# Optimization experiments

Measured on AMD Instinct MI355X. Metric: run time of the kernel, lower is better.

The kernel has to match this reference:

```python
import jax, jax.numpy as jnp
import numpy as np

B, N, D = 2, 8192, 1024
H = 16
HD = D // H  # 64
EPS = 1e-6


def setup_inputs() -> dict:
    key = jax.random.key(0)
    ks = jax.random.split(key, 5)
    scale = 1.0 / np.sqrt(D)
    return {
        "x": jax.random.normal(ks[0], (B, N, D), dtype=jnp.float32),
        "Wq": jax.random.normal(ks[1], (D, D), dtype=jnp.float32) * scale,
        "Wk": jax.random.normal(ks[2], (D, D), dtype=jnp.float32) * scale,
        "Wv": jax.random.normal(ks[3], (D, D), dtype=jnp.float32) * scale,
        "Wo": jax.random.normal(ks[4], (D, D), dtype=jnp.float32) * scale,
    }


def _feature_map(a):
    # ELU + 1 (positive feature map)
    return jax.nn.elu(a) + 1.0


def reference(x, Wq, Wk, Wv, Wo):
    b, n, d = x.shape
    # torch nn.Linear: y = x @ W.T
    q = _feature_map((x @ Wq.T).reshape(b, n, H, HD))  # (B,N,H,hd)
    k = _feature_map((x @ Wk.T).reshape(b, n, H, HD))
    v = (x @ Wv.T).reshape(b, n, H, HD)
    # global kv state per head: (B,H,hd,hd)
    kv = jnp.einsum('bnhd,bnhm->bhdm', k, v)
    k_sum = k.sum(axis=1)  # (B,H,hd)
    numerator = jnp.einsum('bnhd,bhdm->bnhm', q, kv)  # (B,N,H,hd)
    denominator = jnp.einsum('bnhd,bhd->bnh', q, k_sum)[..., None]
    out = numerator / (denominator + EPS)
    out = out.reshape(b, n, d)
    return out @ Wo.T
```

## Files before the change

### kernel.cpp

```cpp
#include <hip/hip_runtime.h>
#include <stdint.h>

#define BB 2
#define NN 8192
#define DD 1024
#define KK 1024
#define NHEAD 16
#define HDIM 64
#define KV_CHUNKS 32

using f32x4  = __attribute__((ext_vector_type(4))) float;
using bf16x8 = __attribute__((ext_vector_type(8))) short;

__device__ __forceinline__ unsigned short f2bf(float f) {
  union { float f; unsigned int u; } v; v.f = f;
  unsigned int r = v.u + 0x7fffu + ((v.u >> 16) & 1u);
  return (unsigned short)(r >> 16);
}
__device__ __forceinline__ float bf2f(unsigned short u) {
  union { unsigned int u; float f; } v; v.u = ((unsigned int)u) << 16;
  return v.f;
}

__device__ __forceinline__ void gload_lds16(const unsigned short* g, unsigned short* l) {
  __builtin_amdgcn_global_load_lds(
      (__attribute__((address_space(1))) void*)(const_cast<unsigned short*>(g)),
      (__attribute__((address_space(3))) void*)(l), 16, 0, 0);
}

__global__ __launch_bounds__(256) void f32_to_bf16_k(const float* __restrict__ in,
                                                     unsigned short* __restrict__ out) {
  size_t i = ((size_t)blockIdx.x * 256 + threadIdx.x) * 8;
  float4 a = *(const float4*)(in + i);
  float4 b = *(const float4*)(in + i + 4);
  uint32_t p0 = (uint32_t)f2bf(a.x) | ((uint32_t)f2bf(a.y) << 16);
  uint32_t p1 = (uint32_t)f2bf(a.z) | ((uint32_t)f2bf(a.w) << 16);
  uint32_t p2 = (uint32_t)f2bf(b.x) | ((uint32_t)f2bf(b.y) << 16);
  uint32_t p3 = (uint32_t)f2bf(b.z) | ((uint32_t)f2bf(b.w) << 16);
  *(uint4*)(out + i) = make_uint4(p0, p1, p2, p3);
}

#define BAR  __builtin_amdgcn_s_barrier()
#define SB   __builtin_amdgcn_sched_barrier(0)
#define WLG  asm volatile("s_waitcnt lgkmcnt(0)" ::: "memory")
#define WVM4 asm volatile("s_waitcnt vmcnt(4)" ::: "memory")
#define WVM0 asm volatile("s_waitcnt vmcnt(0)" ::: "memory")

template <int EPI>
__global__ __launch_bounds__(512, 2) void gemm256(const unsigned short* __restrict__ A,
                                                  const unsigned short* __restrict__ Bw,
                                                  unsigned short* __restrict__ O0,
                                                  unsigned short* __restrict__ O1,
                                                  unsigned short* __restrict__ O2,
                                                  float* __restrict__ OF) {
  __shared__ unsigned short lds[2][2][2][128 * 64];
  const int t = threadIdx.x;
  const int lane = t & 63;
  const int w = t >> 6;
  const int wm = w >> 2;
  const int wn = w & 3;
  const int frow = lane & 15;
  const int g = lane >> 4;
  const int fx = frow & 7;
  const int rowBase = blockIdx.x * 256;
  const int colBase = blockIdx.y * 256;

  const int srow0 = t >> 3;
  const int ssw = ((t & 7) ^ (srow0 & 7)) * 8;
  const unsigned short* sA0 = A + (size_t)(rowBase + srow0) * KK + ssw;
  const unsigned short* sA1 = A + (size_t)(rowBase + 64 + srow0) * KK + ssw;
  const unsigned short* sB0 = Bw + (size_t)(colBase + srow0) * KK + ssw;
  const unsigned short* sB1 = Bw + (size_t)(colBase + 64 + srow0) * KK + ssw;

#define STAGE(db, ab, half, kt)                                                        \
  do {                                                                                 \
    gload_lds16(((ab) ? sB0 : sA0) + (size_t)(half) * 128 * KK + (size_t)(kt) * 64,    \
                &lds[db][ab][half][(0 * 512 + w * 64) * 8]);                           \
    gload_lds16(((ab) ? sB1 : sA1) + (size_t)(half) * 128 * KK + (size_t)(kt) * 64,    \
                &lds[db][ab][half][(1 * 512 + w * 64) * 8]);                           \
  } while (0)

  bf16x8 ar[4][2], br[4][2];
  f32x4 acc[8][4];
#pragma unroll
  for (int i = 0; i < 8; ++i)
#pragma unroll
    for (int j = 0; j < 4; ++j) acc[i][j] = (f32x4){0.f, 0.f, 0.f, 0.f};

#define LDA4(db, mih)                                                                  \
  _Pragma("unroll") for (int mi2 = 0; mi2 < 4; ++mi2)                                  \
  _Pragma("unroll") for (int kk2 = 0; kk2 < 2; ++kk2)                                  \
    ar[mi2][kk2] = *(const bf16x8*)((const char*)&lds[db][0][wm][0] +                  \
        ((mih) * 64 + mi2 * 16 + frow) * 128 + ((kk2 * 4 + g) ^ fx) * 16);

#define LDB2(db, nih)                                                                  \
  _Pragma("unroll") for (int ni2 = 0; ni2 < 2; ++ni2)                                  \
  _Pragma("unroll") for (int kk2 = 0; kk2 < 2; ++kk2)                                  \
    br[(nih) * 2 + ni2][kk2] = *(const bf16x8*)((const char*)&lds[db][1][wn >> 1][0] + \
        ((wn & 1) * 64 + (nih) * 32 + ni2 * 16 + frow) * 128 + ((kk2 * 4 + g) ^ fx) * 16);

#define MFMAQ(mih, nih)                                                                \
  __builtin_amdgcn_s_setprio(1);                                                      \
  _Pragma("unroll") for (int mi2 = 0; mi2 < 4; ++mi2)                                  \
  _Pragma("unroll") for (int ni2 = 0; ni2 < 2; ++ni2)                                  \
  _Pragma("unroll") for (int kk2 = 0; kk2 < 2; ++kk2)                                  \
    acc[(mih) * 4 + mi2][(nih) * 2 + ni2] = __builtin_amdgcn_mfma_f32_16x16x32_bf16(   \
        ar[mi2][kk2], br[(nih) * 2 + ni2][kk2],                                        \
        acc[(mih) * 4 + mi2][(nih) * 2 + ni2], 0, 0, 0);                               \
  __builtin_amdgcn_s_setprio(0);

  STAGE(0, 1, 0, 0); STAGE(0, 1, 1, 0);
  STAGE(0, 0, 0, 0); STAGE(0, 0, 1, 0);
  STAGE(1, 1, 0, 1); STAGE(1, 1, 1, 1);
  WVM4; BAR; SB;

#pragma unroll 1
  for (int i = 0; i < 8; ++i) {
    const bool full = (i < 7);
    const int kt1 = 2 * i + 1, kt2 = 2 * i + 2, kt3 = 2 * i + 3;
    LDA4(0, 0); LDB2(0, 0);
    STAGE(1, 0, 0, kt1);
    BAR; WLG; SB; MFMAQ(0, 0); BAR; SB;
    LDB2(0, 1);
    STAGE(1, 0, 1, kt1);
    BAR; WLG; SB; MFMAQ(0, 1); BAR; SB;
    LDA4(0, 1);
    if (full) STAGE(0, 1, 0, kt2);
    BAR; WLG; SB; MFMAQ(1, 0); BAR; SB;
    if (full) { STAGE(0, 1, 1, kt2); WVM4; } else { WVM0; }
    BAR; SB; MFMAQ(1, 1); BAR; SB;
    LDA4(1, 0); LDB2(1, 0);
    if (full) STAGE(0, 0, 0, kt2);
    BAR; WLG; SB; MFMAQ(0, 0); BAR; SB;
    LDB2(1, 1);
    if (full) STAGE(0, 0, 1, kt2);
    BAR; WLG; SB; MFMAQ(0, 1); BAR; SB;
    LDA4(1, 1);
    if (full) STAGE(1, 1, 0, kt3);
    BAR; WLG; SB; MFMAQ(1, 0); BAR; SB;
    if (full) { STAGE(1, 1, 1, kt3); WVM4; }
    BAR; SB; MFMAQ(1, 1); BAR; SB;
  }

  const int r0 = rowBase + wm * 128 + g * 4;
  if constexpr (EPI == 0) {
    const int ymat = blockIdx.y >> 2;
    unsigned short* dst = (ymat == 0) ? O0 : ((ymat == 1) ? O1 : O2);
    const int c0 = (blockIdx.y & 3) * 256 + wn * 64 + frow;
    const bool doElu = (ymat < 2);
#pragma unroll
    for (int mi = 0; mi < 8; ++mi)
#pragma unroll
      for (int j = 0; j < 4; ++j) {
        const size_t ro = (size_t)(r0 + mi * 16 + j) * DD;
#pragma unroll
        for (int ni = 0; ni < 4; ++ni) {
          float v = acc[mi][ni][j];
          if (doElu) v = (v > 0.f) ? (v + 1.f) : __expf(v);
          dst[ro + c0 + ni * 16] = f2bf(v);
        }
      }
  } else {
    const int c0 = colBase + wn * 64 + frow;
#pragma unroll
    for (int mi = 0; mi < 8; ++mi)
#pragma unroll
      for (int j = 0; j < 4; ++j) {
        const size_t ro = (size_t)(r0 + mi * 16 + j) * DD;
#pragma unroll
        for (int ni = 0; ni < 4; ++ni)
          OF[ro + c0 + ni * 16] = acc[mi][ni][j];
      }
  }
#undef STAGE
#undef LDA4
#undef LDB2
#undef MFMAQ
}

__global__ __launch_bounds__(256) void kv_partial(const unsigned short* __restrict__ Kb,
                                                  const unsigned short* __restrict__ Vb,
                                                  float* __restrict__ kvp,
                                                  float* __restrict__ ksp) {
  __shared__ unsigned short ks[16][64];
  __shared__ float vsf[16][64];
  const int blk = blockIdx.x;
  const int c = blk % KV_CHUNKS;
  const int h = (blk / KV_CHUNKS) % NHEAD;
  const int b = blk / (KV_CHUNKS * NHEAD);
  const int chunkLen = NN / KV_CHUNKS;
  const int t = threadIdx.x;
  const int d = t >> 2;
  const int mq = (t & 3) * 16;
  float acc[16] = {};
  float sk = 0.f;
  const size_t base = ((size_t)b * NN + (size_t)c * chunkLen) * DD + h * HDIM;
  const int half = t >> 7;
  const int tt = t & 127;
  const int rr = tt >> 3;
  const int cc = (tt & 7) * 8;
  const unsigned short* src0 = (half ? Vb : Kb) + base + (size_t)rr * DD + cc;
  for (int n0 = 0; n0 < chunkLen; n0 += 16) {
    uint4 raw = *(const uint4*)(src0 + (size_t)n0 * DD);
    if (half == 0) {
      *(uint4*)&ks[rr][cc] = raw;
    } else {
      const unsigned short* pr = (const unsigned short*)&raw;
      float4 f0, f1;
      f0.x = bf2f(pr[0]); f0.y = bf2f(pr[1]); f0.z = bf2f(pr[2]); f0.w = bf2f(pr[3]);
      f1.x = bf2f(pr[4]); f1.y = bf2f(pr[5]); f1.z = bf2f(pr[6]); f1.w = bf2f(pr[7]);
      *(float4*)&vsf[rr][cc] = f0;
      *(float4*)&vsf[rr][cc + 4] = f1;
    }
    __syncthreads();
#pragma unroll
    for (int nn = 0; nn < 16; ++nn) {
      float kd = bf2f(ks[nn][d]);
      sk += kd;
      const float4* vrow = (const float4*)&vsf[nn][mq];
#pragma unroll
      for (int j4 = 0; j4 < 4; ++j4) {
        float4 vv = vrow[j4];
        acc[j4 * 4 + 0] += kd * vv.x;
        acc[j4 * 4 + 1] += kd * vv.y;
        acc[j4 * 4 + 2] += kd * vv.z;
        acc[j4 * 4 + 3] += kd * vv.w;
      }
    }
    __syncthreads();
  }
  float* dst = kvp + (size_t)blk * 4096 + d * 64 + mq;
#pragma unroll
  for (int j = 0; j < 16; ++j) dst[j] = acc[j];
  if ((t & 3) == 0) ksp[(size_t)blk * 64 + d] = sk;
}

__global__ __launch_bounds__(256) void kv_final(const float* __restrict__ kvp,
                                                const float* __restrict__ ksp,
                                                unsigned short* __restrict__ kvb) {
  const int bh = blockIdx.x;
  const int t = threadIdx.x;
  __shared__ float kvs[4096];
#pragma unroll
  for (int e0 = 0; e0 < 4096; e0 += 256) {
    float s = 0.f;
    for (int cI = 0; cI < KV_CHUNKS; ++cI)
      s += kvp[((size_t)bh * KV_CHUNKS + cI) * 4096 + e0 + t];
    kvs[e0 + t] = s;
  }
  __syncthreads();
  unsigned short* dst = kvb + (size_t)bh * (96 * 64);
#pragma unroll
  for (int e0 = 0; e0 < 4096; e0 += 256) {
    int e = e0 + t;
    dst[e] = f2bf(kvs[(e & 63) * 64 + (e >> 6)]);
  }
  if (t < 64) {
    float s = 0.f;
    for (int cI = 0; cI < KV_CHUNKS; ++cI)
      s += ksp[((size_t)bh * KV_CHUNKS + cI) * 64 + t];
    dst[64 * 64 + t] = f2bf(s);
  }
  for (int e0 = 65 * 64; e0 < 96 * 64; e0 += 256) {
    int e = e0 + t;
    if (e < 96 * 64) dst[e] = 0;
  }
}

__global__ __launch_bounds__(256) void attn_mfma(const unsigned short* __restrict__ Qb,
                                                 const unsigned short* __restrict__ kvb,
                                                 unsigned short* __restrict__ Ob) {
  __shared__ unsigned short Bs[96 * 64];
  __shared__ unsigned short Qs[64 * 64];
  const int t = threadIdx.x;
  const int lane = t & 63;
  const int w = t >> 6;
  const int bh = blockIdx.y;
  const int b = bh >> 4;
  const int h = bh & 15;
  const int rowBase = blockIdx.x * 64;

  const unsigned short* bsrc = kvb + (size_t)bh * (96 * 64);
#pragma unroll
  for (int r = 0; r < 3; ++r) {
    int ci = r * 256 + t;
    int row = ci >> 3, ch = ci & 7;
    gload_lds16(bsrc + row * 64 + (ch ^ (row & 7)) * 8, Bs + ci * 8);
  }
  const int sr = t >> 3, ch0 = t & 7;
#pragma unroll
  for (int i = 0; i < 2; ++i) {
    int row = i * 32 + sr;
    const unsigned short* src =
        Qb + ((size_t)(b * NN + rowBase + row)) * DD + h * HDIM + (ch0 ^ (row & 7)) * 8;
    gload_lds16(src, Qs + row * 64 + ch0 * 8);
  }
  __syncthreads();

  const int frow = lane & 15;
  const int g = lane >> 4;
  bf16x8 a[2];
#pragma unroll
  for (int kk = 0; kk < 2; ++kk)
    a[kk] = *(const bf16x8*)(Qs + (w * 16 + frow) * 64 + ((kk * 4 + g) ^ (lane & 7)) * 8);

  f32x4 acc[5];
#pragma unroll
  for (int c = 0; c < 5; ++c) acc[c] = (f32x4){0.f, 0.f, 0.f, 0.f};
#pragma unroll
  for (int c = 0; c < 5; ++c) {
#pragma unroll
    for (int kk = 0; kk < 2; ++kk) {
      bf16x8 bf = *(const bf16x8*)(Bs + (c * 16 + frow) * 64 + ((kk * 4 + g) ^ (lane & 7)) * 8);
      acc[c] = __builtin_amdgcn_mfma_f32_16x16x32_bf16(a[kk], bf, acc[c], 0, 0, 0);
    }
  }

  float rden[4];
#pragma unroll
  for (int j = 0; j < 4; ++j) {
    float den = __shfl(acc[4][j], g * 16, 64);
    rden[j] = 1.f / (den + 1e-6f);
  }
  const size_t obase = ((size_t)(b * NN + rowBase + w * 16 + g * 4)) * DD + h * HDIM + frow;
#pragma unroll
  for (int c = 0; c < 4; ++c)
#pragma unroll
    for (int j = 0; j < 4; ++j)
      Ob[obase + (size_t)j * DD + c * 16] = f2bf(acc[c][j] * rden[j]);
}

extern "C" void kernel_launch(void* const* d_in, const int* in_sizes, int n_in,
                              void* d_out, int out_size, void* d_ws, size_t ws_size,
                              hipStream_t stream) {
  const float* x  = (const float*)d_in[0];
  const float* Wq = (const float*)d_in[1];
  const float* Wk = (const float*)d_in[2];
  const float* Wv = (const float*)d_in[3];
  const float* Wo = (const float*)d_in[4];
  float* out = (float*)d_out;

  char* ws = (char*)d_ws;
  size_t off = 0;
  auto alloc = [&](size_t bytes) -> char* {
    char* p = ws + off;
    off += (bytes + 255) & ~(size_t)255;
    return p;
  };
  const size_t xN = (size_t)BB * NN * DD;
  unsigned short* xb   = (unsigned short*)alloc(xN * 2);
  unsigned short* qb   = (unsigned short*)alloc(xN * 2);
  unsigned short* kb   = (unsigned short*)alloc(xN * 2);
  unsigned short* vb   = (unsigned short*)alloc(xN * 2);
  unsigned short* wqkv = (unsigned short*)alloc((size_t)3 * DD * DD * 2);
  unsigned short* wob  = (unsigned short*)alloc((size_t)DD * DD * 2);
  float* ksp = (float*)alloc((size_t)BB * NHEAD * KV_CHUNKS * 64 * 4);
  unsigned short* kvb = (unsigned short*)alloc((size_t)BB * NHEAD * 96 * 64 * 2);
  float* kvp = (float*)xb;
  unsigned short* ob = xb;

  f32_to_bf16_k<<<(int)(xN / (256 * 8)), 256, 0, stream>>>(x, xb);
  f32_to_bf16_k<<<(DD * DD) / (256 * 8), 256, 0, stream>>>(Wq, wqkv);
  f32_to_bf16_k<<<(DD * DD) / (256 * 8), 256, 0, stream>>>(Wk, wqkv + (size_t)DD * DD);
  f32_to_bf16_k<<<(DD * DD) / (256 * 8), 256, 0, stream>>>(Wv, wqkv + (size_t)2 * DD * DD);
  f32_to_bf16_k<<<(DD * DD) / (256 * 8), 256, 0, stream>>>(Wo, wob);

  dim3 gq(64, 12);
  gemm256<0><<<gq, 512, 0, stream>>>(xb, wqkv, qb, kb, vb, nullptr);

  kv_partial<<<BB * NHEAD * KV_CHUNKS, 256, 0, stream>>>(kb, vb, kvp, ksp);
  kv_final<<<BB * NHEAD, 256, 0, stream>>>(kvp, ksp, kvb);

  dim3 ga(NN / 64, BB * NHEAD);
  attn_mfma<<<ga, 256, 0, stream>>>(qb, kvb, ob);

  dim3 go(64, 4);
  gemm256<1><<<go, 512, 0, stream>>>(ob, wob, nullptr, nullptr, nullptr, out);
}
```

Before: 244.6 us.

## Swizzle QKV GEMM block order and use smaller-tile GEMM for output projection

Result: slower. 282.5 us (+15.5%).

```diff
diff --git a/kernel.cpp b/kernel.cpp
--- a/kernel.cpp
+++ b/kernel.cpp
@@ -46,13 +46,11 @@
 #define WVM4 asm volatile("s_waitcnt vmcnt(4)" ::: "memory")
 #define WVM0 asm volatile("s_waitcnt vmcnt(0)" ::: "memory")
 
-template <int EPI>
-__global__ __launch_bounds__(512, 2) void gemm256(const unsigned short* __restrict__ A,
-                                                  const unsigned short* __restrict__ Bw,
-                                                  unsigned short* __restrict__ O0,
-                                                  unsigned short* __restrict__ O1,
-                                                  unsigned short* __restrict__ O2,
-                                                  float* __restrict__ OF) {
+__global__ __launch_bounds__(512, 2) void gemm256_qkv(const unsigned short* __restrict__ A,
+                                                      const unsigned short* __restrict__ Bw,
+                                                      unsigned short* __restrict__ O0,
+                                                      unsigned short* __restrict__ O1,
+                                                      unsigned short* __restrict__ O2) {
   __shared__ unsigned short lds[2][2][2][128 * 64];
   const int t = threadIdx.x;
   const int lane = t & 63;
@@ -62,8 +60,12 @@
   const int frow = lane & 15;
   const int g = lane >> 4;
   const int fx = frow & 7;
-  const int rowBase = blockIdx.x * 256;
-  const int colBase = blockIdx.y * 256;
+  const int id = blockIdx.y * 64 + blockIdx.x;
+  const int swz = (id & 7) * 96 + (id >> 3);
+  const int bx = swz & 63;
+  const int by = swz >> 6;
+  const int rowBase = bx * 256;
+  const int colBase = by * 256;
 
   const int srow0 = t >> 3;
   const int ssw = ((t & 7) ^ (srow0 & 7)) * 8;
@@ -143,39 +145,91 @@
   }
 
   const int r0 = rowBase + wm * 128 + g * 4;
-  if constexpr (EPI == 0) {
-    const int ymat = blockIdx.y >> 2;
-    unsigned short* dst = (ymat == 0) ? O0 : ((ymat == 1) ? O1 : O2);
-    const int c0 = (blockIdx.y & 3) * 256 + wn * 64 + frow;
-    const bool doElu = (ymat < 2);
-#pragma unroll
-    for (int mi = 0; mi < 8; ++mi)
-#pragma unroll
-      for (int j = 0; j < 4; ++j) {
-        const size_t ro = (size_t)(r0 + mi * 16 + j) * DD;
-#pragma unroll
-        for (int ni = 0; ni < 4; ++ni) {
-          float v = acc[mi][ni][j];
-          if (doElu) v = (v > 0.f) ? (v + 1.f) : __expf(v);
-          dst[ro + c0 + ni * 16] = f2bf(v);
-        }
+  const int ymat = by >> 2;
+  unsigned short* dst = (ymat == 0) ? O0 : ((ymat == 1) ? O1 : O2);
+  const int c0 = (by & 3) * 256 + wn * 64 + frow;
+  const bool doElu = (ymat < 2);
+#pragma unroll
+  for (int mi = 0; mi < 8; ++mi)
+#pragma unroll
+    for (int j = 0; j < 4; ++j) {
+      const size_t ro = (size_t)(r0 + mi * 16 + j) * DD;
+#pragma unroll
+      for (int ni = 0; ni < 4; ++ni) {
+        float v = acc[mi][ni][j];
+        if (doElu) v = (v > 0.f) ? (v + 1.f) : __expf(v);
+        dst[ro + c0 + ni * 16] = f2bf(v);
       }
-  } else {
-    const int c0 = colBase + wn * 64 + frow;
-#pragma unroll
-    for (int mi = 0; mi < 8; ++mi)
-#pragma unroll
-      for (int j = 0; j < 4; ++j) {
-        const size_t ro = (size_t)(r0 + mi * 16 + j) * DD;
-#pragma unroll
-        for (int ni = 0; ni < 4; ++ni)
-          OF[ro + c0 + ni * 16] = acc[mi][ni][j];
-      }
-  }
+    }
 #undef STAGE
 #undef LDA4
 #undef LDB2
 #undef MFMAQ
+}
+
+__global__ __launch_bounds__(256, 2) void gemm_bt_f32(const unsigned short* __restrict__ A,
+                                                      const unsigned short* __restrict__ Bw,
+                                                      float* __restrict__ Cp,
+                                                      int M, int N, int K) {
+  constexpr int BM = 128, BN = 128, BK = 64;
+  __shared__ unsigned short As[BM * BK];
+  __shared__ unsigned short Bs[BN * BK];
+  const int t = threadIdx.x;
+  const int lane = t & 63;
+  const int w = t >> 6;
+  const int wr = w >> 1, wc = w & 1;
+  const int id = blockIdx.y * gridDim.x + blockIdx.x;
+  const int swz = (id & 7) * 128 + (id >> 3);
+  const int rowBase = (swz & 127) * BM;
+  const int colBase = (swz >> 7) * BN;
+
+  f32x4 acc[4][4];
+#pragma unroll
+  for (int i = 0; i < 4; ++i)
+#pragma unroll
+    for (int j = 0; j < 4; ++j) acc[i][j] = (f32x4){0.f, 0.f, 0.f, 0.f};
+
+  const int sr = t >> 3;
+  const int sc = (t & 7) * 8;
+  const unsigned short* gA = A + (size_t)(rowBase + sr) * K + sc;
+  const unsigned short* gB = Bw + (size_t)(colBase + sr) * K + sc;
+
+  for (int k0 = 0; k0 < K; k0 += BK) {
+#pragma unroll
+    for (int i = 0; i < 4; ++i) {
+      gload_lds16(gA + (size_t)i * 32 * K + k0, As + (i * 256 + w * 64) * 8);
+      gload_lds16(gB + (size_t)i * 32 * K + k0, Bs + (i * 256 + w * 64) * 8);
+    }
+    __syncthreads();
+#pragma unroll
+    for (int kk = 0; kk < BK; kk += 32) {
+      bf16x8 af[4], bfv[4];
+#pragma unroll
+      for (int mi = 0; mi < 4; ++mi)
+        af[mi] = *(const bf16x8*)(As + (wr * 64 + mi * 16 + (lane & 15)) * BK + kk + (lane >> 4) * 8);
+#pragma unroll
+      for (int ni = 0; ni < 4; ++ni)
+        bfv[ni] = *(const bf16x8*)(Bs + (wc * 64 + ni * 16 + (lane & 15)) * BK + kk + (lane >> 4) * 8);
+#pragma unroll
+      for (int mi = 0; mi < 4; ++mi)
+#pragma unroll
+        for (int ni = 0; ni < 4; ++ni)
+          acc[mi][ni] = __builtin_amdgcn_mfma_f32_16x16x32_bf16(af[mi], bfv[ni], acc[mi][ni], 0, 0, 0);
+    }
+    __syncthreads();
+  }
+
+  const int r0 = rowBase + wr * 64 + ((lane >> 4) << 2);
+  const int c0 = colBase + wc * 64 + (lane & 15);
+#pragma unroll
+  for (int mi = 0; mi < 4; ++mi)
+#pragma unroll
+    for (int j = 0; j < 4; ++j) {
+      const size_t rowOff = (size_t)(r0 + mi * 16 + j) * N;
+#pragma unroll
+      for (int ni = 0; ni < 4; ++ni)
+        Cp[rowOff + c0 + ni * 16] = acc[mi][ni][j];
+    }
 }
 
 __global__ __launch_bounds__(256) void kv_partial(const unsigned short* __restrict__ Kb,
@@ -366,7 +420,7 @@
   f32_to_bf16_k<<<(DD * DD) / (256 * 8), 256, 0, stream>>>(Wo, wob);
 
   dim3 gq(64, 12);
-  gemm256<0><<<gq, 512, 0, stream>>>(xb, wqkv, qb, kb, vb, nullptr);
+  gemm256_qkv<<<gq, 512, 0, stream>>>(xb, wqkv, qb, kb, vb);
 
   kv_partial<<<BB * NHEAD * KV_CHUNKS, 256, 0, stream>>>(kb, vb, kvp, ksp);
   kv_final<<<BB * NHEAD, 256, 0, stream>>>(kvp, ksp, kvb);
@@ -374,6 +428,6 @@
   dim3 ga(NN / 64, BB * NHEAD);
   attn_mfma<<<ga, 256, 0, stream>>>(qb, kvb, ob);
 
-  dim3 go(64, 4);
-  gemm256<1><<<go, 512, 0, stream>>>(ob, wob, nullptr, nullptr, nullptr, out);
-}
+  dim3 go(128, 8);
+  gemm_bt_f32<<<go, 256, 0, stream>>>(ob, wob, out, BB * NN, DD, DD);
+}
```
